# Optimization experiments

Hardware: AMD Instinct MI355X
Metric: run time of the kernel (lower is better)

Reference implementation:

```python
import jax, jax.numpy as jnp
import numpy as np

RES = 64

TRI_TABLE = jnp.array([
    [-1,-1,-1,-1,-1,-1],[1,0,2,-1,-1,-1],[4,0,3,-1,-1,-1],[1,4,2,1,3,4],
    [3,1,5,-1,-1,-1],[2,3,0,2,5,3],[1,4,0,1,5,4],[4,2,5,-1,-1,-1],
    [4,5,2,-1,-1,-1],[4,1,0,4,5,1],[3,2,0,3,5,2],[1,3,5,-1,-1,-1],
    [4,1,2,4,3,1],[3,0,4,-1,-1,-1],[2,0,1,-1,-1,-1],[-1,-1,-1,-1,-1,-1]], dtype=jnp.int32)
NUM_TRI = jnp.array([0,1,1,2,1,2,2,1,1,2,2,1,2,1,1,0], dtype=jnp.int32)
BASE_EDGES = jnp.array([0,1,0,2,0,3,1,2,1,3,2,3], dtype=jnp.int32)


def _make_tet_grid(res):
    # Kuhn 6-tet decomposition of each cube of a (res+1)^3 grid.
    n = res + 1
    ii, jj, kk = np.meshgrid(np.arange(n), np.arange(n), np.arange(n), indexing='ij')
    verts = (np.stack([ii, jj, kk], -1).reshape(-1, 3).astype(np.float32)) / res
    def vid(i, j, k):
        return (i * n + j) * n + k
    i, j, k = np.meshgrid(np.arange(res), np.arange(res), np.arange(res), indexing='ij')
    i, j, k = i.ravel(), j.ravel(), k.ravel()
    c = [vid(i + (b & 1), j + ((b >> 1) & 1), k + ((b >> 2) & 1)) for b in range(8)]
    kuhn = [(0,1,3,7),(0,3,2,7),(0,2,6,7),(0,6,4,7),(0,4,5,7),(0,5,1,7)]
    tets = np.stack([np.stack([c[a], c[b], c[d], c[e]], -1) for (a, b, d, e) in kuhn], 1)
    return verts, tets.reshape(-1, 4).astype(np.int64)


def setup_inputs() -> dict:
    key = jax.random.key(0)
    verts, tets = _make_tet_grid(RES)
    level = jax.random.normal(key, (verts.shape[0], 1), dtype=jnp.float32)
    return {"level": level, "pos": jnp.asarray(verts), "tet": jnp.asarray(tets), "threshold": 0}


def reference(level, pos, tet, threshold):
    sdf = level - threshold                    # [N,1]
    occ = sdf[:, 0] > 0                        # [N]
    occ_fx4 = occ[tet]                         # [F,4]
    occ_sum = occ_fx4.sum(-1)
    valid = (occ_sum > 0) & (occ_sum < 4)
    vt = tet[valid]                            # [Fv,4]
    occ_valid = occ_fx4[valid]                 # [Fv,4]

    edges = jnp.sort(vt[:, BASE_EDGES].reshape(-1, 2), axis=1)   # [Fv*6,2]
    unique_edges, idx_map = jnp.unique(edges, axis=0, return_inverse=True)
    idx_map = idx_map.reshape(-1)
    mask_edges = occ[unique_edges].sum(-1) == 1                  # crossing edges
    mapping = jnp.where(mask_edges, jnp.cumsum(mask_edges) - 1, -1)
    idx_map = mapping[idx_map].reshape(-1, 6)                    # [Fv,6]
    interp_v = unique_edges[mask_edges]                          # [M,2]

    p = pos[interp_v]                                            # [M,2,3]
    s = sdf[interp_v][..., 0] * jnp.array([1.0, -1.0], dtype=sdf.dtype)  # [M,2]
    w = s[:, ::-1] / s.sum(1, keepdims=True)                     # flip / denom
    verts_out = (p * w[..., None]).sum(1)                        # [M,3]

    v_id = 2 ** jnp.arange(4, dtype=jnp.int32)
    tetindex = (occ_valid.astype(jnp.int32) * v_id).sum(-1)      # [Fv]
    num_tri = NUM_TRI[tetindex]
    m1, m2 = num_tri == 1, num_tri == 2
    f1 = jnp.take_along_axis(idx_map[m1], TRI_TABLE[tetindex[m1]][:, :3], axis=1).reshape(-1, 3)
    f2 = jnp.take_along_axis(idx_map[m2], TRI_TABLE[tetindex[m2]][:, :6], axis=1).reshape(-1, 3)
    faces = jnp.concatenate([f1, f2], axis=0)
    return verts_out, faces
```

## Files before the change

kernel.cpp:

```cpp
#include <hip/hip_runtime.h>


#define RESX 64
#define NV   65
#define NV2  4225
#define NVERT 274625
#define NCUBE 262144
#define BLOCK 256
#define NBLK 1073
#define CBLK 1024
#define WINW 20

__constant__ int c_tri[16][6] = {
    {-1,-1,-1,-1,-1,-1},{1,0,2,-1,-1,-1},{4,0,3,-1,-1,-1},{1,4,2,1,3,4},
    {3,1,5,-1,-1,-1},{2,3,0,2,5,3},{1,4,0,1,5,4},{4,2,5,-1,-1,-1},
    {4,5,2,-1,-1,-1},{4,1,0,4,5,1},{3,2,0,3,5,2},{1,3,5,-1,-1,-1},
    {4,1,2,4,3,1},{3,0,4,-1,-1,-1},{2,0,1,-1,-1,-1},{-1,-1,-1,-1,-1,-1}};
__constant__ int c_ntri[16] = {0,1,1,2,1,2,2,1,1,2,2,1,2,1,1,0};
__constant__ int c_kuhn[6][4] = {{0,1,3,7},{0,3,2,7},{0,2,6,7},{0,6,4,7},{0,4,5,7},{0,5,1,7}};
__constant__ int c_off8[8] = {0,4225,65,4290,1,4226,66,4291};
__constant__ int c_loc[6][6] = {
    {0,0,0,1,1,3},{0,0,0,2,3,2},{0,0,0,2,2,6},
    {0,0,0,4,6,4},{0,0,0,4,4,5},{0,0,0,1,5,1}};
__constant__ int c_dir[6][6] = {
    {3,5,6,1,2,0},{5,1,6,3,0,4},{1,2,6,0,4,3},
    {2,0,6,1,3,5},{0,4,6,3,5,1},{4,3,6,0,1,2}};

__device__ __forceinline__ unsigned block_reduce(unsigned v, unsigned* lds) {
    int tid = threadIdx.x, lane = tid & 63, w = tid >> 6;
#pragma unroll
    for (int off = 32; off > 0; off >>= 1)
        v += (unsigned)__shfl_xor((int)v, off, 64);
    if (lane == 0) lds[w] = v;
    __syncthreads();
    if (tid == 0) lds[4] = lds[0] + lds[1] + lds[2] + lds[3];
    __syncthreads();
    return lds[4];
}

__device__ __forceinline__ unsigned block_scan_excl(unsigned val, unsigned* lds,
                                                    unsigned& block_total) {
    int tid = threadIdx.x, lane = tid & 63, w = tid >> 6;
    unsigned x = val;
#pragma unroll
    for (int off = 1; off < 64; off <<= 1) {
        unsigned y = (unsigned)__shfl_up((int)x, off, 64);
        if (lane >= off) x += y;
    }
    if (lane == 63) lds[w] = x;
    __syncthreads();
    if (tid == 0) {
        unsigned s = 0;
#pragma unroll
        for (int i = 0; i < 4; i++) { unsigned t = lds[i]; lds[i + 4] = s; s += t; }
        lds[8] = s;
    }
    __syncthreads();
    block_total = lds[8];
    return x - val + lds[4 + w];
}

__global__ void __launch_bounds__(256)
pass1(const float* __restrict__ level, const float* __restrict__ thrp,
      unsigned char* __restrict__ flagsArr, unsigned short* __restrict__ locEx,
      unsigned* __restrict__ bsE, unsigned* __restrict__ bsT) {
    __shared__ unsigned lds[9];
    __shared__ unsigned ldsc[5];
    int tid = threadIdx.x;
    int bid = blockIdx.x;
    int gid = bid * BLOCK + tid;
    float thr = thrp[0];

    unsigned fl = 0;
    if (gid < NVERT) {
        int i = gid / NV2; int r = gid - i * NV2; int j = r / NV; int k = r - j * NV;
        bool okx = i < RESX, oky = j < RESX, okz = k < RESX;
        float v0 = level[gid] - thr;
        bool s0 = v0 > 0.f;
        fl = s0 ? 0x80u : 0u;
        const int b2d[8] = {0, 3, 1, 5, 0, 4, 2, 6};
#pragma unroll
        for (int b = 1; b < 8; b++) {
            bool ok = (!(b & 1) || okx) && (!(b & 2) || oky) && (!(b & 4) || okz);
            if (ok) {
                float vb = level[gid + c_off8[b]] - thr;
                if ((vb > 0.f) != s0) fl |= (1u << b2d[b]);
            }
        }
        flagsArr[gid] = (unsigned char)fl;
    }
    unsigned cnt = __popc(fl & 0x7fu);
    unsigned totE;
    unsigned ex = block_scan_excl(cnt, lds, totE);
    if (gid < NVERT) locEx[gid] = (unsigned short)ex;
    if (tid == 0) bsE[bid] = totE;

    unsigned tv = 0;
    if (gid < NCUBE) {
        int ci = gid >> 12, cj = (gid >> 6) & 63, ck = gid & 63;
        int base = (ci * NV + cj) * NV + ck;
        unsigned occ8 = 0;
#pragma unroll
        for (int b = 0; b < 8; b++)
            occ8 |= ((level[base + c_off8[b]] - thr) > 0.f ? 1u : 0u) << b;
        unsigned c1 = 0, c2 = 0;
#pragma unroll
        for (int t = 0; t < 6; t++) {
            int cfg = ((occ8 >> c_kuhn[t][0]) & 1) | (((occ8 >> c_kuhn[t][1]) & 1) << 1)
                    | (((occ8 >> c_kuhn[t][2]) & 1) << 2) | (((occ8 >> c_kuhn[t][3]) & 1) << 3);
            int nt = c_ntri[cfg];
            c1 += (nt == 1); c2 += (nt == 2);
        }
        tv = c1 | (c2 << 16);
    }
    unsigned totC = block_reduce(tv, ldsc);
    if (tid == 0) bsT[bid] = totC;
}

__global__ void __launch_bounds__(256)
pass2(const float* __restrict__ level, const float* __restrict__ thrp,
      const unsigned char* __restrict__ flagsArr,
      const unsigned short* __restrict__ locEx,
      const unsigned* __restrict__ bsE, const unsigned* __restrict__ bsT,
      float* __restrict__ out) {
    __shared__ unsigned lds[9];
    __shared__ unsigned ldsc[5];
    __shared__ unsigned pEw[WINW];
    int tid = threadIdx.x;
    int bid = blockIdx.x;
    int gid = bid * BLOCK + tid;
    float thr = thrp[0];

    int g0 = bid << 8;
    int wci = g0 >> 12, wcj = (g0 >> 6) & 63;
    int base0 = (wci * NV + wcj) * NV;
    int wb = (bid < CBLK) ? (base0 >> 8) : 0;

    unsigned lE = 0, lEp = 0, lWb = 0, l1 = 0, l1p = 0, l2p = 0;
    for (int t = tid; t < NBLK; t += BLOCK) {
        unsigned e = bsE[t], c = bsT[t];
        lE += e; l1 += c & 0xffffu;
        if (t < bid) { lEp += e; l1p += c & 0xffffu; l2p += c >> 16; }
        if (t < wb)  { lWb += e; }
    }
    unsigned M    = block_reduce(lE,  ldsc);
    unsigned pE   = block_reduce(lEp, ldsc);
    unsigned C1   = block_reduce(l1,  ldsc);
    unsigned p1b  = block_reduce(l1p, ldsc);
    unsigned p2b  = block_reduce(l2p, ldsc);
    unsigned wAcc = block_reduce(lWb, ldsc);
    if (tid < WINW) {
        unsigned s = wAcc;
        for (int d = 0; d < tid; d++) {
            int t = wb + d;
            s += (t < NBLK) ? bsE[t] : 0u;
        }
        pEw[tid] = s;
    }
    __syncthreads();

    if (gid < NVERT) {
        unsigned fl = flagsArr[gid];
        if (fl & 0x7fu) {
            int i = gid / NV2; int r = gid - i * NV2; int j = r / NV; int k = r - j * NV;
            float v0 = level[gid] - thr;
            unsigned rank = pE + locEx[gid];
            const float inv = 1.f / 64.f;
            const int d2b[7] = {4, 2, 6, 1, 5, 3, 7};
            float fi = (float)i, fj = (float)j, fk = (float)k;
#pragma unroll
            for (int d = 0; d < 7; d++) {
                if (fl & (1u << d)) {
                    const int b = d2b[d];
                    float s1 = level[gid + c_off8[b]] - thr;
                    float denom = v0 - s1;
                    float w0 = (-s1) / denom;
                    float w1 = v0 / denom;
                    float* o = out + 3u * rank;
                    o[0] = (fi * w0 + (fi + (float)(b & 1)) * w1) * inv;
                    o[1] = (fj * w0 + (fj + (float)((b >> 1) & 1)) * w1) * inv;
                    o[2] = (fk * w0 + (fk + (float)((b >> 2) & 1)) * w1) * inv;
                    rank++;
                }
            }
        }
    }

    if (bid >= CBLK) return;
    int ci = gid >> 12, cj = (gid >> 6) & 63, ck = gid & 63;
    int base = (ci * NV + cj) * NV + ck;
    unsigned long long f8 = 0ull;
#pragma unroll
    for (int b = 0; b < 8; b++)
        f8 |= (unsigned long long)flagsArr[base + c_off8[b]] << (8 * b);
    unsigned occ8 = 0;
#pragma unroll
    for (int b = 0; b < 8; b++) occ8 |= (unsigned)((f8 >> (8 * b + 7)) & 1ull) << b;
    int cfgs[6], nts[6];
    unsigned c1 = 0, c2 = 0;
#pragma unroll
    for (int t = 0; t < 6; t++) {
        int cfg = ((occ8 >> c_kuhn[t][0]) & 1) | (((occ8 >> c_kuhn[t][1]) & 1) << 1)
                | (((occ8 >> c_kuhn[t][2]) & 1) << 2) | (((occ8 >> c_kuhn[t][3]) & 1) << 3);
        cfgs[t] = cfg;
        int nt = c_ntri[cfg];
        nts[t] = nt;
        c1 += (nt == 1); c2 += (nt == 2);
    }
    unsigned tot2;
    unsigned ex2 = block_scan_excl(c1 | (c2 << 16), lds, tot2);
    unsigned p1 = p1b + (ex2 & 0xffffu);
    unsigned p2 = p2b + (ex2 >> 16);
    float* of = out + 3ull * M;
#pragma unroll
    for (int t = 0; t < 6; t++) {
        int nt = nts[t];
        if (nt == 0) continue;
        int cfg = cfgs[t];
        unsigned tri0 = (nt == 1) ? p1 : (C1 + 2u * p2);
        int cntm = 3 * nt;
        for (int m = 0; m < cntm; m++) {
            int e = c_tri[cfg][m];
            int lc = c_loc[t][e];
            int dir = c_dir[t][e];
            int lo = base + c_off8[lc];
            unsigned flb = (unsigned)((f8 >> (8 * lc)) & 0xffull);
            unsigned rnk = pEw[(lo >> 8) - wb] + locEx[lo]
                         + __popc(flb & ((1u << dir) - 1u));
            of[3u * tri0 + (unsigned)m] = (float)rnk;
        }
        p1 += (nt == 1);
        p2 += (nt == 2);
    }
}

extern "C" void kernel_launch(void* const* d_in, const int* in_sizes, int n_in,
                              void* d_out, int out_size, void* d_ws, size_t ws_size,
                              hipStream_t stream) {
    const float* level = (const float*)d_in[0];
    const float* thrp = (const float*)d_in[3];
    float* out = (float*)d_out;

    char* p = (char*)d_ws;
    unsigned char* flagsArr = (unsigned char*)p;
    p += (NVERT + 255) & ~255;
    unsigned short* locEx = (unsigned short*)p;
    p += ((sizeof(unsigned short) * NVERT) + 255) & ~255;
    unsigned* bsE = (unsigned*)p;  p += sizeof(unsigned) * NBLK;
    unsigned* bsT = (unsigned*)p;

    pass1<<<NBLK, BLOCK, 0, stream>>>(level, thrp, flagsArr, locEx, bsE, bsT);
    pass2<<<NBLK, BLOCK, 0, stream>>>(level, thrp, flagsArr, locEx, bsE, bsT, out);
}
```

Before: 123.4 us.

## Split output pass into vertex and face kernels with LDS-staged coalesced stores

The combined pass2 is split into two kernels, one writing interpolated vertices and one writing face indices. Each kernel stages its outputs in shared memory and then writes them to global memory as contiguous, coalesced nontemporal stores, replacing the scattered per-thread stores. This adds a kernel launch and a large LDS allocation per block, which may lower occupancy. It also assumes per-block output counts fit the fixed LDS buffers.

```diff
diff --git a/kernel.cpp b/kernel.cpp
--- a/kernel.cpp
+++ b/kernel.cpp
@@ -118,33 +118,80 @@
 }
 
 __global__ void __launch_bounds__(256)
-pass2(const float* __restrict__ level, const float* __restrict__ thrp,
-      const unsigned char* __restrict__ flagsArr,
-      const unsigned short* __restrict__ locEx,
-      const unsigned* __restrict__ bsE, const unsigned* __restrict__ bsT,
-      float* __restrict__ out) {
-    __shared__ unsigned lds[9];
+pass2v(const float* __restrict__ level, const float* __restrict__ thrp,
+       const unsigned char* __restrict__ flagsArr,
+       const unsigned short* __restrict__ locEx,
+       const unsigned* __restrict__ bsE, float* __restrict__ out) {
     __shared__ unsigned ldsc[5];
-    __shared__ unsigned pEw[WINW];
+    __shared__ float ldsV[1792 * 3];
     int tid = threadIdx.x;
     int bid = blockIdx.x;
     int gid = bid * BLOCK + tid;
     float thr = thrp[0];
 
+    unsigned lEp = 0;
+    for (int t = tid; t < bid; t += BLOCK) lEp += bsE[t];
+    unsigned pE = block_reduce(lEp, ldsc);
+    unsigned totE = bsE[bid];
+
+    if (gid < NVERT) {
+        unsigned fl = flagsArr[gid];
+        if (fl & 0x7fu) {
+            int i = gid / NV2; int r = gid - i * NV2; int j = r / NV; int k = r - j * NV;
+            float v0 = level[gid] - thr;
+            unsigned slot = locEx[gid];
+            const float inv = 1.f / 64.f;
+            const int d2b[7] = {4, 2, 6, 1, 5, 3, 7};
+            float fi = (float)i, fj = (float)j, fk = (float)k;
+#pragma unroll
+            for (int d = 0; d < 7; d++) {
+                if (fl & (1u << d)) {
+                    const int b = d2b[d];
+                    float s1 = level[gid + c_off8[b]] - thr;
+                    float denom = v0 - s1;
+                    float w0 = (-s1) / denom;
+                    float w1 = v0 / denom;
+                    float* o = &ldsV[3u * slot];
+                    o[0] = (fi * w0 + (fi + (float)(b & 1)) * w1) * inv;
+                    o[1] = (fj * w0 + (fj + (float)((b >> 1) & 1)) * w1) * inv;
+                    o[2] = (fk * w0 + (fk + (float)((b >> 2) & 1)) * w1) * inv;
+                    slot++;
+                }
+            }
+        }
+    }
+    __syncthreads();
+    float* dst = out + 3u * pE;
+    unsigned n = totE * 3u;
+    for (unsigned idx = tid; idx < n; idx += BLOCK)
+        __builtin_nontemporal_store(ldsV[idx], &dst[idx]);
+}
+
+__global__ void __launch_bounds__(256)
+pass2f(const unsigned char* __restrict__ flagsArr,
+       const unsigned short* __restrict__ locEx,
+       const unsigned* __restrict__ bsE, const unsigned* __restrict__ bsT,
+       float* __restrict__ out) {
+    __shared__ unsigned lds[9];
+    __shared__ unsigned ldsc[5];
+    __shared__ unsigned pEw[WINW];
+    __shared__ float ldsF[1536 * 6];
+    int tid = threadIdx.x;
+    int bid = blockIdx.x;
+    int gid = bid * BLOCK + tid;
+
     int g0 = bid << 8;
     int wci = g0 >> 12, wcj = (g0 >> 6) & 63;
-    int base0 = (wci * NV + wcj) * NV;
-    int wb = (bid < CBLK) ? (base0 >> 8) : 0;
-
-    unsigned lE = 0, lEp = 0, lWb = 0, l1 = 0, l1p = 0, l2p = 0;
+    int wb = ((wci * NV + wcj) * NV) >> 8;
+
+    unsigned lE = 0, lWb = 0, l1 = 0, l1p = 0, l2p = 0;
     for (int t = tid; t < NBLK; t += BLOCK) {
         unsigned e = bsE[t], c = bsT[t];
         lE += e; l1 += c & 0xffffu;
-        if (t < bid) { lEp += e; l1p += c & 0xffffu; l2p += c >> 16; }
+        if (t < bid) { l1p += c & 0xffffu; l2p += c >> 16; }
         if (t < wb)  { lWb += e; }
     }
     unsigned M    = block_reduce(lE,  ldsc);
-    unsigned pE   = block_reduce(lEp, ldsc);
     unsigned C1   = block_reduce(l1,  ldsc);
     unsigned p1b  = block_reduce(l1p, ldsc);
     unsigned p2b  = block_reduce(l2p, ldsc);
@@ -159,34 +206,6 @@
     }
     __syncthreads();
 
-    if (gid < NVERT) {
-        unsigned fl = flagsArr[gid];
-        if (fl & 0x7fu) {
-            int i = gid / NV2; int r = gid - i * NV2; int j = r / NV; int k = r - j * NV;
-            float v0 = level[gid] - thr;
-            unsigned rank = pE + locEx[gid];
-            const float inv = 1.f / 64.f;
-            const int d2b[7] = {4, 2, 6, 1, 5, 3, 7};
-            float fi = (float)i, fj = (float)j, fk = (float)k;
-#pragma unroll
-            for (int d = 0; d < 7; d++) {
-                if (fl & (1u << d)) {
-                    const int b = d2b[d];
-                    float s1 = level[gid + c_off8[b]] - thr;
-                    float denom = v0 - s1;
-                    float w0 = (-s1) / denom;
-                    float w1 = v0 / denom;
-                    float* o = out + 3u * rank;
-                    o[0] = (fi * w0 + (fi + (float)(b & 1)) * w1) * inv;
-                    o[1] = (fj * w0 + (fj + (float)((b >> 1) & 1)) * w1) * inv;
-                    o[2] = (fk * w0 + (fk + (float)((b >> 2) & 1)) * w1) * inv;
-                    rank++;
-                }
-            }
-        }
-    }
-
-    if (bid >= CBLK) return;
     int ci = gid >> 12, cj = (gid >> 6) & 63, ck = gid & 63;
     int base = (ci * NV + cj) * NV + ck;
     unsigned long long f8 = 0ull;
@@ -209,15 +228,17 @@
     }
     unsigned tot2;
     unsigned ex2 = block_scan_excl(c1 | (c2 << 16), lds, tot2);
-    unsigned p1 = p1b + (ex2 & 0xffffu);
-    unsigned p2 = p2b + (ex2 >> 16);
-    float* of = out + 3ull * M;
+    unsigned f1 = tot2 & 0xffffu;
+    unsigned f2 = tot2 >> 16;
+    unsigned l1c = ex2 & 0xffffu;
+    unsigned l2c = ex2 >> 16;
+    unsigned n1 = f1 * 3u;
 #pragma unroll
     for (int t = 0; t < 6; t++) {
         int nt = nts[t];
         if (nt == 0) continue;
         int cfg = cfgs[t];
-        unsigned tri0 = (nt == 1) ? p1 : (C1 + 2u * p2);
+        unsigned basef = (nt == 1) ? (3u * l1c) : (n1 + 6u * l2c);
         int cntm = 3 * nt;
         for (int m = 0; m < cntm; m++) {
             int e = c_tri[cfg][m];
@@ -227,11 +248,20 @@
             unsigned flb = (unsigned)((f8 >> (8 * lc)) & 0xffull);
             unsigned rnk = pEw[(lo >> 8) - wb] + locEx[lo]
                          + __popc(flb & ((1u << dir) - 1u));
-            of[3u * tri0 + (unsigned)m] = (float)rnk;
-        }
-        p1 += (nt == 1);
-        p2 += (nt == 2);
-    }
+            ldsF[basef + (unsigned)m] = (float)rnk;
+        }
+        l1c += (nt == 1);
+        l2c += (nt == 2);
+    }
+    __syncthreads();
+    float* of = out + 3ull * M;
+    float* o1 = of + 3u * p1b;
+    for (unsigned idx = tid; idx < n1; idx += BLOCK)
+        __builtin_nontemporal_store(ldsF[idx], &o1[idx]);
+    unsigned n2 = f2 * 6u;
+    float* o2 = of + 3u * (C1 + 2u * p2b);
+    for (unsigned idx = tid; idx < n2; idx += BLOCK)
+        __builtin_nontemporal_store(ldsF[n1 + idx], &o2[idx]);
 }
 
 extern "C" void kernel_launch(void* const* d_in, const int* in_sizes, int n_in,
@@ -250,5 +280,6 @@
     unsigned* bsT = (unsigned*)p;
 
     pass1<<<NBLK, BLOCK, 0, stream>>>(level, thrp, flagsArr, locEx, bsE, bsT);
-    pass2<<<NBLK, BLOCK, 0, stream>>>(level, thrp, flagsArr, locEx, bsE, bsT, out);
-}
+    pass2v<<<NBLK, BLOCK, 0, stream>>>(level, thrp, flagsArr, locEx, bsE, out);
+    pass2f<<<CBLK, BLOCK, 0, stream>>>(flagsArr, locEx, bsE, bsT, out);
+}
```

After: 120.1 us. 1.03x faster.
